# Optimization experiments

Measured on AMD Instinct MI355X. Metric: run time of the kernel, lower is better.

## Reference

```python
import jax, jax.numpy as jnp
import numpy as np

NA = 100000
NB = 100000
N_REL = 6
REL_SRC = ['A', 'B', 'A', 'B', 'A', 'B']
REL_DST = ['B', 'A', 'A', 'B', 'B', 'A']
N_NODES = {'A': NA, 'B': NB}
H_DIM, OUT_DIM, N_BASES, N_EDGES = 64, 16, 4, 500000


def setup_inputs() -> dict:
    key = jax.random.key(0)
    ks = jax.random.split(key, 16)
    inp = {
        'embed_A': jax.random.normal(ks[0], (NA, H_DIM), jnp.float32) * 0.1,
        'embed_B': jax.random.normal(ks[1], (NB, H_DIM), jnp.float32) * 0.1,
        'bias0': jnp.zeros((H_DIM,), jnp.float32),
        'w_comp1': jax.random.normal(ks[2], (N_REL, N_BASES), jnp.float32) * 0.5,
        'basis1': jax.random.normal(ks[3], (N_BASES, H_DIM, H_DIM), jnp.float32) * (1.0 / np.sqrt(H_DIM)),
        'bias1': jnp.zeros((H_DIM,), jnp.float32),
        'w_comp2': jax.random.normal(ks[4], (N_REL, N_BASES), jnp.float32) * 0.5,
        'basis2': jax.random.normal(ks[5], (N_BASES, H_DIM, OUT_DIM), jnp.float32) * (1.0 / np.sqrt(H_DIM)),
        'bias2': jnp.zeros((OUT_DIM,), jnp.float32),
    }
    for r in range(N_REL):
        inp[f'src_r{r}'] = jax.random.randint(ks[6 + r], (N_EDGES,), 0, N_NODES[REL_SRC[r]], jnp.int32)
        inp[f'dst_r{r}'] = jax.random.randint(jax.random.fold_in(ks[6 + r], 7), (N_EDGES,), 0, N_NODES[REL_DST[r]], jnp.int32)
    return inp


def _hetero_conv(h, W_rels, bias, edges, out_dim, activation):
    # h: dict ntype -> [N, d_in]; W_rels: None or [n_rel, d_in, d_out]
    out = {nt: jnp.zeros((N_NODES[nt], out_dim), h['A'].dtype) for nt in N_NODES}
    for r in range(N_REL):
        src_t, dst_t = REL_SRC[r], REL_DST[r]
        src, dst = edges[r]
        x = h[src_t] if W_rels is None else h[src_t] @ W_rels[r]  # [N_src, d_out]
        msg = x[src]  # gather: [E, d_out]
        n_dst = N_NODES[dst_t]
        agg = jax.ops.segment_sum(msg, dst, num_segments=n_dst)
        deg = jax.ops.segment_sum(jnp.ones((msg.shape[0],), msg.dtype), dst, num_segments=n_dst)
        out[dst_t] = out[dst_t] + agg / jnp.maximum(deg, 1.0)[:, None]  # norm='right'
    out = {nt: out[nt] + bias for nt in out}
    if activation is not None:
        out = {nt: activation(out[nt]) for nt in out}
    return out


def reference(embed_A, embed_B, bias0, w_comp1, basis1, bias1, w_comp2, basis2, bias2,
              src_r0, dst_r0, src_r1, dst_r1, src_r2, dst_r2,
              src_r3, dst_r3, src_r4, dst_r4, src_r5, dst_r5):
    edges = [(src_r0, dst_r0), (src_r1, dst_r1), (src_r2, dst_r2),
             (src_r3, dst_r3), (src_r4, dst_r4), (src_r5, dst_r5)]
    h = {'A': embed_A, 'B': embed_B}
    # layer 0: weight=False -> pure normalized aggregation + bias + relu
    h = _hetero_conv(h, None, bias0, edges, H_DIM, jax.nn.relu)
    # hidden layer with basis-decomposed weights
    W1 = jnp.einsum('rb,bio->rio', w_comp1, basis1)
    h = _hetero_conv(h, W1, bias1, edges, H_DIM, jax.nn.relu)
    # output layer, no activation
    W2 = jnp.einsum('rb,bio->rio', w_comp2, basis2)
    h = _hetero_conv(h, W2, bias2, edges, OUT_DIM, None)
    return h['A']  # logits for category node type
```

## Files before the change

kernel.cpp:

```cpp
#include <hip/hip_runtime.h>

#define NN 100000
#define EE 500000
#define DD 64
#define OD 16
#define NR 6
#define NBASE 4
#define BSH 10
#define NBK 98
#define SBLK 128
#define FLATN (NBK * SBLK)
#define STCAP 5632
#define DBIN 64
#define LROW 100

struct Edges { const int* src[NR]; const int* dst[NR]; };

typedef __attribute__((ext_vector_type(8))) short bf16x8;
typedef __attribute__((ext_vector_type(4))) float f32x4;

__device__ __forceinline__ float bf2f(ushort u) {
    union { unsigned int i; float f; } v; v.i = ((unsigned int)u) << 16; return v.f;
}
__device__ __forceinline__ ushort f2bf(float f) {
    unsigned int x = __float_as_uint(f);
    unsigned int r = (x + 0x7fffu + ((x >> 16) & 1u)) >> 16;
    return (ushort)r;
}
__device__ __forceinline__ void bfpair(unsigned int u, float& lo, float& hi) {
    lo = __uint_as_float(u << 16);
    hi = __uint_as_float(u & 0xffff0000u);
}

__global__ __launch_bounds__(256) void build_w_kernel(
    const float* __restrict__ wc1, const float* __restrict__ b1,
    const float* __restrict__ wc2, const float* __restrict__ b2,
    ushort* __restrict__ Wp1, ushort* __restrict__ Wp2)
{
    int idx = blockIdx.x * blockDim.x + threadIdx.x;
    const int n1 = NR * DD * DD;
    const int n2 = NR * DD * OD;
    if (idx < n1) {
        int r = idx >> 12, rem = idx & 4095;
        int i = rem >> 6, o = rem & 63;
        float s = 0.f;
        #pragma unroll
        for (int b = 0; b < NBASE; ++b) s += wc1[r * NBASE + b] * b1[b * 4096 + rem];
        Wp1[(((size_t)(r * 8 + (i >> 3)) * 64 + o) << 3) + (i & 7)] = f2bf(s);
    } else if (idx < n1 + n2) {
        int j = idx - n1;
        int r = j >> 10, rem = j & 1023;
        int i = rem >> 4, o = rem & 15;
        float s = 0.f;
        #pragma unroll
        for (int b = 0; b < NBASE; ++b) s += wc2[r * NBASE + b] * b2[b * 1024 + rem];
        Wp2[(((size_t)(r * 8 + (i >> 3)) * 16 + o) << 3) + (i & 7)] = f2bf(s);
    }
}

__global__ __launch_bounds__(256) void count_kernel(Edges ep, int* __restrict__ cnt_mat)
{
    __shared__ int h[NBK];
    int r = blockIdx.y, blk = blockIdx.x;
    const int* __restrict__ dst = ep.dst[r];
    const int chunk = (EE + SBLK - 1) / SBLK;
    int e0 = blk * chunk, e1 = min(e0 + chunk, EE);
    for (int i = threadIdx.x; i < NBK; i += 256) h[i] = 0;
    __syncthreads();
    for (int e = e0 + threadIdx.x; e < e1; e += 256)
        atomicAdd(&h[dst[e] >> BSH], 1);
    __syncthreads();
    for (int b = threadIdx.x; b < NBK; b += 256)
        cnt_mat[r * FLATN + b * SBLK + blk] = h[b];
}

__global__ __launch_bounds__(1024) void flat_scan_kernel(
    const int* __restrict__ cnt_mat, int* __restrict__ off_flat, int* __restrict__ bbase)
{
    __shared__ int wsum[16];
    const int TPE = 13;
    int r = blockIdx.x;
    int tid = threadIdx.x, lane = tid & 63, wid = tid >> 6;
    int base = tid * TPE;
    int v[TPE];
    int s = 0;
    #pragma unroll
    for (int j = 0; j < TPE; ++j) {
        int i = base + j;
        v[j] = (i < FLATN) ? cnt_mat[r * FLATN + i] : 0;
        s += v[j];
    }
    int si = s;
    #pragma unroll
    for (int off = 1; off < 64; off <<= 1) {
        int t = __shfl_up(si, off);
        if (lane >= off) si += t;
    }
    if (lane == 63) wsum[wid] = si;
    __syncthreads();
    if (wid == 0) {
        int ws = (lane < 16) ? wsum[lane] : 0;
        #pragma unroll
        for (int off = 1; off < 16; off <<= 1) {
            int t = __shfl_up(ws, off);
            if (lane >= off) ws += t;
        }
        if (lane < 16) wsum[lane] = ws;
    }
    __syncthreads();
    int texcl = (wid > 0 ? wsum[wid - 1] : 0) + (si - s);
    int part = 0;
    #pragma unroll
    for (int j = 0; j < TPE; ++j) {
        int i = base + j;
        if (i < FLATN) {
            int o = texcl + part;
            off_flat[r * FLATN + i] = o;
            if ((i & (SBLK - 1)) == 0) bbase[r * (NBK + 1) + (i >> 7)] = o;
        }
        part += v[j];
    }
    if (tid == 0) bbase[r * (NBK + 1) + NBK] = EE;
}

__global__ __launch_bounds__(256) void scatter2_kernel(
    Edges ep, const int* __restrict__ off_flat, unsigned int* __restrict__ ebuf)
{
    __shared__ int goff[NBK];
    __shared__ int lcnt[NBK];
    int r = blockIdx.y, blk = blockIdx.x;
    const int* __restrict__ src = ep.src[r];
    const int* __restrict__ dst = ep.dst[r];
    unsigned int* eb = ebuf + (size_t)r * EE;
    const int chunk = (EE + SBLK - 1) / SBLK;
    int e0 = blk * chunk, e1 = min(e0 + chunk, EE);
    if (threadIdx.x < NBK) {
        goff[threadIdx.x] = off_flat[r * FLATN + threadIdx.x * SBLK + blk];
        lcnt[threadIdx.x] = 0;
    }
    __syncthreads();
    for (int e = e0 + threadIdx.x; e < e1; e += 256) {
        int d = dst[e];
        int b = d >> BSH;
        int pos = goff[b] + atomicAdd(&lcnt[b], 1);
        eb[pos] = (unsigned int)src[e] | ((unsigned int)(d & 1023) << 17);
    }
}

__global__ __launch_bounds__(256) void csr_fine_kernel(
    const unsigned int* __restrict__ ebuf, const int* __restrict__ bbase,
    int* __restrict__ row_ptr, float* __restrict__ inv_deg, int* __restrict__ col_idx)
{
    __shared__ int nh[1024];
    __shared__ int nb[1024];
    __shared__ int wsum4[4];
    __shared__ int stage[STCAP];
    int r = blockIdx.y, b = blockIdx.x;
    int tid = threadIdx.x, lane = tid & 63, wid = tid >> 6;
    int gb = bbase[r * (NBK + 1) + b];
    int ge = bbase[r * (NBK + 1) + b + 1];
    int cnt = ge - gb;
    if (cnt > STCAP) cnt = STCAP;
    const unsigned int* eb = ebuf + (size_t)r * EE + gb;
    #pragma unroll
    for (int j = 0; j < 4; ++j) nh[tid * 4 + j] = 0;
    __syncthreads();
    for (int i = tid; i < cnt; i += 256)
        atomicAdd(&nh[(eb[i] >> 17) & 1023], 1);
    __syncthreads();
    int v0 = nh[tid * 4 + 0], v1 = nh[tid * 4 + 1], v2 = nh[tid * 4 + 2], v3 = nh[tid * 4 + 3];
    int s = v0 + v1 + v2 + v3;
    int si = s;
    #pragma unroll
    for (int off = 1; off < 64; off <<= 1) {
        int t = __shfl_up(si, off);
        if (lane >= off) si += t;
    }
    if (lane == 63) wsum4[wid] = si;
    __syncthreads();
    if (tid == 0) {
        int a = 0;
        #pragma unroll
        for (int k = 0; k < 4; ++k) { int t = wsum4[k]; wsum4[k] = a; a += t; }
    }
    __syncthreads();
    int texcl = wsum4[wid] + (si - s);
    int p0 = texcl, p1 = p0 + v0, p2 = p1 + v1, p3 = p2 + v2;
    nb[tid * 4 + 0] = p0; nb[tid * 4 + 1] = p1; nb[tid * 4 + 2] = p2; nb[tid * 4 + 3] = p3;
    {
        int node0 = b * 1024 + tid * 4;
        int pj[4] = { p0, p1, p2, p3 };
        int vj[4] = { v0, v1, v2, v3 };
        #pragma unroll
        for (int j = 0; j < 4; ++j) {
            int node = node0 + j;
            if (node < NN) {
                row_ptr[r * (NN + 1) + node] = gb + pj[j];
                inv_deg[r * NN + node] = 1.0f / (float)(vj[j] > 1 ? vj[j] : 1);
            }
        }
    }
    if (b == NBK - 1 && tid == 0) row_ptr[r * (NN + 1) + NN] = EE;
    #pragma unroll
    for (int j = 0; j < 4; ++j) nh[tid * 4 + j] = 0;
    __syncthreads();
    for (int i = tid; i < cnt; i += 256) {
        unsigned int w = eb[i];
        int loc = (w >> 17) & 1023;
        int pos = nb[loc] + atomicAdd(&nh[loc], 1);
        stage[pos] = (int)(w & 0x1ffffu);
    }
    __syncthreads();
    int* co = col_idx + (size_t)r * EE + gb;
    for (int i = tid; i < cnt; i += 256) co[i] = stage[i];
}

__device__ __forceinline__ int sdeg(int vr, int n, const int* __restrict__ rp)
{
    if (vr == 0)
        return (rp[1 * (NN + 1) + n + 1] - rp[1 * (NN + 1) + n])
             + (rp[2 * (NN + 1) + n + 1] - rp[2 * (NN + 1) + n])
             + (rp[5 * (NN + 1) + n + 1] - rp[5 * (NN + 1) + n]);
    return (rp[0 * (NN + 1) + n + 1] - rp[0 * (NN + 1) + n])
         + (rp[3 * (NN + 1) + n + 1] - rp[3 * (NN + 1) + n])
         + (rp[4 * (NN + 1) + n + 1] - rp[4 * (NN + 1) + n]);
}

__global__ __launch_bounds__(256) void bsort_kernel(
    const int* __restrict__ row_ptr, int* __restrict__ perm, int* __restrict__ iperm)
{
    __shared__ int h[DBIN];
    __shared__ int base_[DBIN];
    int vr = blockIdx.y, b = blockIdx.x;
    int n0 = b * 1024;
    int cnt = min(1024, NN - n0);
    int tid = threadIdx.x;
    if (tid < DBIN) h[tid] = 0;
    __syncthreads();
    int bin[4];
    #pragma unroll
    for (int j = 0; j < 4; ++j) {
        int i = tid + j * 256;
        if (i < cnt) {
            bin[j] = min(sdeg(vr, n0 + i, row_ptr), DBIN - 1);
            atomicAdd(&h[bin[j]], 1);
        } else bin[j] = -1;
    }
    __syncthreads();
    if (tid < 64) {
        int v = h[tid];
        int s = v;
        #pragma unroll
        for (int off = 1; off < 64; off <<= 1) {
            int t = __shfl_up(s, off);
            if (tid >= off) s += t;
        }
        base_[tid] = s - v;
        h[tid] = 0;
    }
    __syncthreads();
    #pragma unroll
    for (int j = 0; j < 4; ++j) {
        if (bin[j] >= 0) {
            int n = n0 + tid + j * 256;
            int pos = n0 + base_[bin[j]] + atomicAdd(&h[bin[j]], 1);
            perm[vr * NN + pos] = n;
            iperm[vr * NN + n] = pos;
        }
    }
}

__global__ __launch_bounds__(256) void translate_kernel(
    const int* __restrict__ iperm, int* __restrict__ col_idx)
{
    const int srcSide[NR] = {0, 1, 0, 1, 0, 1};
    int r = blockIdx.y;
    const int* ip = iperm + srcSide[r] * NN;
    int* ci = col_idx + (size_t)r * EE;
    for (int e = blockIdx.x * 256 + threadIdx.x; e < EE; e += gridDim.x * 256)
        ci[e] = ip[ci[e]];
}

__global__ __launch_bounds__(256) void cvtp_kernel(
    const float* __restrict__ inA, const float* __restrict__ inB,
    const int* __restrict__ perm, ushort* __restrict__ outA, ushort* __restrict__ outB)
{
    int side = blockIdx.y;
    int t = blockIdx.x * 256 + threadIdx.x;
    if (t >= NN * 8) return;
    int idx = t >> 3, j = t & 7;
    int n = perm[side * NN + idx];
    const float* in = side ? inB : inA;
    ushort* out = side ? outB : outA;
    float4 v0 = ((const float4*)in)[n * 16 + j * 2];
    float4 v1 = ((const float4*)in)[n * 16 + j * 2 + 1];
    int4 o;
    o.x = (int)((unsigned int)f2bf(v0.x) | ((unsigned int)f2bf(v0.y) << 16));
    o.y = (int)((unsigned int)f2bf(v0.z) | ((unsigned int)f2bf(v0.w) << 16));
    o.z = (int)((unsigned int)f2bf(v1.x) | ((unsigned int)f2bf(v1.y) << 16));
    o.w = (int)((unsigned int)f2bf(v1.z) | ((unsigned int)f2bf(v1.w) << 16));
    *(int4*)(out + (size_t)idx * DD + j * 8) = o;
}

__global__ __launch_bounds__(256) void layer0_kernel(
    const ushort* __restrict__ eA, const ushort* __restrict__ eB,
    const int* __restrict__ row_ptr, const int* __restrict__ col_idx,
    const float* __restrict__ inv_deg, const int* __restrict__ perm,
    const float* __restrict__ bias, ushort* __restrict__ hA, ushort* __restrict__ hB)
{
    int side = blockIdx.y;
    const int relT[2][3] = { {1, 2, 5}, {0, 3, 4} };
    int tid = threadIdx.x;
    int wid = tid >> 6, lane = tid & 63;
    int grp = lane >> 3, sub = lane & 7;
    int idx = blockIdx.x * 32 + wid * 8 + grp;
    bool valid = (idx < NN);
    int n = valid ? perm[side * NN + idx] : 0;
    float acc[8];
    {
        float4 b0 = *(const float4*)(bias + sub * 8);
        float4 b1 = *(const float4*)(bias + sub * 8 + 4);
        acc[0] = b0.x; acc[1] = b0.y; acc[2] = b0.z; acc[3] = b0.w;
        acc[4] = b1.x; acc[5] = b1.y; acc[6] = b1.z; acc[7] = b1.w;
    }
    #pragma unroll
    for (int ks = 0; ks < 3; ++ks) {
        int r = relT[side][ks];
        const ushort* F = ((side == 0) == (ks == 1)) ? eA : eB;
        const int* rp = row_ptr + r * (NN + 1);
        const int* ci = col_idx + (size_t)r * EE;
        int s = valid ? rp[n] : 0;
        int e = valid ? rp[n + 1] : 0;
        float a0 = 0.f, a1 = 0.f, a2 = 0.f, a3 = 0.f, a4 = 0.f, a5 = 0.f, a6 = 0.f, a7 = 0.f;
        int t = s;
        for (; t + 2 <= e; t += 2) {
            int c0 = ci[t], c1 = ci[t + 1];
            int4 u = *(const int4*)(F + (size_t)c0 * DD + sub * 8);
            int4 w = *(const int4*)(F + (size_t)c1 * DD + sub * 8);
            float l, h;
            bfpair((unsigned int)u.x, l, h); a0 += l; a1 += h;
            bfpair((unsigned int)u.y, l, h); a2 += l; a3 += h;
            bfpair((unsigned int)u.z, l, h); a4 += l; a5 += h;
            bfpair((unsigned int)u.w, l, h); a6 += l; a7 += h;
            bfpair((unsigned int)w.x, l, h); a0 += l; a1 += h;
            bfpair((unsigned int)w.y, l, h); a2 += l; a3 += h;
            bfpair((unsigned int)w.z, l, h); a4 += l; a5 += h;
            bfpair((unsigned int)w.w, l, h); a6 += l; a7 += h;
        }
        if (t < e) {
            int4 u = *(const int4*)(F + (size_t)ci[t] * DD + sub * 8);
            float l, h;
            bfpair((unsigned int)u.x, l, h); a0 += l; a1 += h;
            bfpair((unsigned int)u.y, l, h); a2 += l; a3 += h;
            bfpair((unsigned int)u.z, l, h); a4 += l; a5 += h;
            bfpair((unsigned int)u.w, l, h); a6 += l; a7 += h;
        }
        float inv = valid ? inv_deg[r * NN + n] : 0.f;
        acc[0] += a0 * inv; acc[1] += a1 * inv; acc[2] += a2 * inv; acc[3] += a3 * inv;
        acc[4] += a4 * inv; acc[5] += a5 * inv; acc[6] += a6 * inv; acc[7] += a7 * inv;
    }
    if (valid) {
        ushort* h = side ? hB : hA;
        int4 o;
        o.x = (int)((unsigned int)f2bf(fmaxf(acc[0], 0.f)) | ((unsigned int)f2bf(fmaxf(acc[1], 0.f)) << 16));
        o.y = (int)((unsigned int)f2bf(fmaxf(acc[2], 0.f)) | ((unsigned int)f2bf(fmaxf(acc[3], 0.f)) << 16));
        o.z = (int)((unsigned int)f2bf(fmaxf(acc[4], 0.f)) | ((unsigned int)f2bf(fmaxf(acc[5], 0.f)) << 16));
        o.w = (int)((unsigned int)f2bf(fmaxf(acc[6], 0.f)) | ((unsigned int)f2bf(fmaxf(acc[7], 0.f)) << 16));
        *(int4*)(h + (size_t)idx * DD + sub * 8) = o;
    }
}

__global__ __launch_bounds__(256) void layer1_fused_kernel(
    const ushort* __restrict__ h0A, const ushort* __restrict__ h0B,
    const int* __restrict__ row_ptr, const int* __restrict__ col_idx,
    const float* __restrict__ inv_deg, const int* __restrict__ perm,
    const ushort* __restrict__ Wp, const float* __restrict__ bias,
    ushort* __restrict__ h1A, ushort* __restrict__ h1B)
{
    __shared__ unsigned int sZ[32 * LROW];
    int side = blockIdx.y;
    const int relT[2][3] = { {1, 2, 5}, {0, 3, 4} };
    int tid = threadIdx.x;
    int wid = tid >> 6, lane = tid & 63;
    int grp = lane >> 3, sub = lane & 7;
    int ln = wid * 8 + grp;
    int idx0 = blockIdx.x * 32;
    int idx = idx0 + ln;
    bool valid = (idx < NN);
    int n = valid ? perm[side * NN + idx] : 0;
    #pragma unroll
    for (int ks = 0; ks < 3; ++ks) {
        int r = relT[side][ks];
        const ushort* F = ((side == 0) == (ks == 1)) ? h0A : h0B;
        const int* rp = row_ptr + r * (NN + 1);
        const int* ci = col_idx + (size_t)r * EE;
        int s = valid ? rp[n] : 0;
        int e = valid ? rp[n + 1] : 0;
        float a0 = 0.f, a1 = 0.f, a2 = 0.f, a3 = 0.f, a4 = 0.f, a5 = 0.f, a6 = 0.f, a7 = 0.f;
        int t = s;
        for (; t + 2 <= e; t += 2) {
            int c0 = ci[t], c1 = ci[t + 1];
            int4 u = *(const int4*)(F + (size_t)c0 * DD + sub * 8);
            int4 w = *(const int4*)(F + (size_t)c1 * DD + sub * 8);
            float l, h;
            bfpair((unsigned int)u.x, l, h); a0 += l; a1 += h;
            bfpair((unsigned int)u.y, l, h); a2 += l; a3 += h;
            bfpair((unsigned int)u.z, l, h); a4 += l; a5 += h;
            bfpair((unsigned int)u.w, l, h); a6 += l; a7 += h;
            bfpair((unsigned int)w.x, l, h); a0 += l; a1 += h;
            bfpair((unsigned int)w.y, l, h); a2 += l; a3 += h;
            bfpair((unsigned int)w.z, l, h); a4 += l; a5 += h;
            bfpair((unsigned int)w.w, l, h); a6 += l; a7 += h;
        }
        if (t < e) {
            int4 u = *(const int4*)(F + (size_t)ci[t] * DD + sub * 8);
            float l, h;
            bfpair((unsigned int)u.x, l, h); a0 += l; a1 += h;
            bfpair((unsigned int)u.y, l, h); a2 += l; a3 += h;
            bfpair((unsigned int)u.z, l, h); a4 += l; a5 += h;
            bfpair((unsigned int)u.w, l, h); a6 += l; a7 += h;
        }
        float inv = valid ? inv_deg[r * NN + n] : 0.f;
        int4 o;
        o.x = (int)((unsigned int)f2bf(a0 * inv) | ((unsigned int)f2bf(a1 * inv) << 16));
        o.y = (int)((unsigned int)f2bf(a2 * inv) | ((unsigned int)f2bf(a3 * inv) << 16));
        o.z = (int)((unsigned int)f2bf(a4 * inv) | ((unsigned int)f2bf(a5 * inv) << 16));
        o.w = (int)((unsigned int)f2bf(a6 * inv) | ((unsigned int)f2bf(a7 * inv) << 16));
        *(int4*)&sZ[ln * LROW + ks * 32 + sub * 4] = o;
    }
    __syncthreads();
    int q = lane & 15, p = lane >> 4;
    int base16 = (wid >> 1) * 16, cb = (wid & 1) * 32;
    f32x4 acc0 = {0.f, 0.f, 0.f, 0.f};
    f32x4 acc1 = {0.f, 0.f, 0.f, 0.f};
    #pragma unroll
    for (int ks = 0; ks < 3; ++ks) {
        int rel = relT[side][ks];
        #pragma unroll
        for (int tt = 0; tt < 2; ++tt) {
            int4 t4 = *(const int4*)&sZ[(base16 + q) * LROW + (ks * 2 + tt) * 16 + p * 4];
            bf16x8 a = *(const bf16x8*)&t4;
            const ushort* wb = Wp + (((size_t)(rel * 8 + tt * 4 + p) * 64 + cb + q) << 3);
            bf16x8 b0 = *(const bf16x8*)wb;
            bf16x8 b1 = *(const bf16x8*)(wb + 16 * 8);
            acc0 = __builtin_amdgcn_mfma_f32_16x16x32_bf16(a, b0, acc0, 0, 0, 0);
            acc1 = __builtin_amdgcn_mfma_f32_16x16x32_bf16(a, b1, acc1, 0, 0, 0);
        }
    }
    __syncthreads();
    ushort* sC = (ushort*)sZ;
    {
        float bv0 = bias[cb + q], bv1 = bias[cb + 16 + q];
        #pragma unroll
        for (int v = 0; v < 4; ++v) {
            int row = base16 + p * 4 + v;
            sC[row * 64 + cb + q]      = f2bf(fmaxf(acc0[v] + bv0, 0.f));
            sC[row * 64 + cb + 16 + q] = f2bf(fmaxf(acc1[v] + bv1, 0.f));
        }
    }
    __syncthreads();
    ushort* out = side ? h1B : h1A;
    int row = tid >> 3, c8 = (tid & 7) * 8;
    if (idx0 + row < NN)
        *(int4*)(out + (size_t)(idx0 + row) * DD + c8) = *(const int4*)(sC + row * 64 + c8);
}

__global__ __launch_bounds__(256) void layer2_fused_kernel(
    const ushort* __restrict__ h1A, const ushort* __restrict__ h1B,
    const int* __restrict__ row_ptr, const int* __restrict__ col_idx,
    const float* __restrict__ inv_deg, const int* __restrict__ perm,
    const ushort* __restrict__ Wp, const float* __restrict__ bias,
    float* __restrict__ out)
{
    __shared__ unsigned int sZ[32 * LROW];
    const int relT[3] = { 1, 2, 5 };
    int tid = threadIdx.x;
    int wid = tid >> 6, lane = tid & 63;
    int grp = lane >> 3, sub = lane & 7;
    int ln = wid * 8 + grp;
    int idx0 = blockIdx.x * 32;
    int idx = idx0 + ln;
    bool valid = (idx < NN);
    int n = valid ? perm[idx] : 0;
    #pragma unroll
    for (int ks = 0; ks < 3; ++ks) {
        int r = relT[ks];
        const ushort* F = (ks == 1) ? h1A : h1B;
        const int* rp = row_ptr + r * (NN + 1);
        const int* ci = col_idx + (size_t)r * EE;
        int s = valid ? rp[n] : 0;
        int e = valid ? rp[n + 1] : 0;
        float a0 = 0.f, a1 = 0.f, a2 = 0.f, a3 = 0.f, a4 = 0.f, a5 = 0.f, a6 = 0.f, a7 = 0.f;
        int t = s;
        for (; t + 2 <= e; t += 2) {
            int c0 = ci[t], c1 = ci[t + 1];
            int4 u = *(const int4*)(F + (size_t)c0 * DD + sub * 8);
            int4 w = *(const int4*)(F + (size_t)c1 * DD + sub * 8);
            float l, h;
            bfpair((unsigned int)u.x, l, h); a0 += l; a1 += h;
            bfpair((unsigned int)u.y, l, h); a2 += l; a3 += h;
            bfpair((unsigned int)u.z, l, h); a4 += l; a5 += h;
            bfpair((unsigned int)u.w, l, h); a6 += l; a7 += h;
            bfpair((unsigned int)w.x, l, h); a0 += l; a1 += h;
            bfpair((unsigned int)w.y, l, h); a2 += l; a3 += h;
            bfpair((unsigned int)w.z, l, h); a4 += l; a5 += h;
            bfpair((unsigned int)w.w, l, h); a6 += l; a7 += h;
        }
        if (t < e) {
            int4 u = *(const int4*)(F + (size_t)ci[t] * DD + sub * 8);
            float l, h;
            bfpair((unsigned int)u.x, l, h); a0 += l; a1 += h;
            bfpair((unsigned int)u.y, l, h); a2 += l; a3 += h;
            bfpair((unsigned int)u.z, l, h); a4 += l; a5 += h;
            bfpair((unsigned int)u.w, l, h); a6 += l; a7 += h;
        }
        float inv = valid ? inv_deg[r * NN + n] : 0.f;
        int4 o;
        o.x = (int)((unsigned int)f2bf(a0 * inv) | ((unsigned int)f2bf(a1 * inv) << 16));
        o.y = (int)((unsigned int)f2bf(a2 * inv) | ((unsigned int)f2bf(a3 * inv) << 16));
        o.z = (int)((unsigned int)f2bf(a4 * inv) | ((unsigned int)f2bf(a5 * inv) << 16));
        o.w = (int)((unsigned int)f2bf(a6 * inv) | ((unsigned int)f2bf(a7 * inv) << 16));
        *(int4*)&sZ[ln * LROW + ks * 32 + sub * 4] = o;
    }
    __syncthreads();
    if (wid < 2) {
        int q = lane & 15, p = lane >> 4;
        int base16 = wid * 16;
        f32x4 acc = {0.f, 0.f, 0.f, 0.f};
        #pragma unroll
        for (int ks = 0; ks < 3; ++ks) {
            int rel = relT[ks];
            #pragma unroll
            for (int tt = 0; tt < 2; ++tt) {
                int4 t4 = *(const int4*)&sZ[(base16 + q) * LROW + (ks * 2 + tt) * 16 + p * 4];
                bf16x8 a = *(const bf16x8*)&t4;
                bf16x8 b = *(const bf16x8*)(Wp + (((size_t)(rel * 8 + tt * 4 + p) * 16 + q) << 3));
                acc = __builtin_amdgcn_mfma_f32_16x16x32_bf16(a, b, acc, 0, 0, 0);
            }
        }
        float bv = bias[q];
        #pragma unroll
        for (int v = 0; v < 4; ++v) {
            int ridx = idx0 + base16 + p * 4 + v;
            if (ridx < NN) {
                int pn = perm[ridx];
                out[(size_t)pn * OD + q] = acc[v] + bv;
            }
        }
    }
}

extern "C" void kernel_launch(void* const* d_in, const int* in_sizes, int n_in,
                              void* d_out, int out_size, void* d_ws, size_t ws_size,
                              hipStream_t stream)
{
    const float* embA  = (const float*)d_in[0];
    const float* embB  = (const float*)d_in[1];
    const float* bias0 = (const float*)d_in[2];
    const float* wc1   = (const float*)d_in[3];
    const float* b1    = (const float*)d_in[4];
    const float* bias1 = (const float*)d_in[5];
    const float* wc2   = (const float*)d_in[6];
    const float* b2    = (const float*)d_in[7];
    const float* bias2 = (const float*)d_in[8];

    Edges ep;
    for (int r = 0; r < NR; ++r) {
        ep.src[r] = (const int*)d_in[9 + 2 * r];
        ep.dst[r] = (const int*)d_in[10 + 2 * r];
    }

    char* ws = (char*)d_ws;
    size_t off = 0;
    auto alloc = [&](size_t bytes) {
        void* p = ws + off;
        off = (off + bytes + 255) & ~(size_t)255;
        return p;
    };
    ushort* Wp1     = (ushort*)alloc((size_t)NR * 8 * 64 * 8 * 2);
    ushort* Wp2     = (ushort*)alloc((size_t)NR * 8 * 16 * 8 * 2);
    int*    cnt_mat = (int*)   alloc((size_t)NR * FLATN * 4);
    int*    off_fl  = (int*)   alloc((size_t)NR * FLATN * 4);
    int*    bbase   = (int*)   alloc((size_t)NR * (NBK + 1) * 4);
    int*    row_ptr = (int*)   alloc((size_t)NR * (NN + 1) * 4);
    float*  inv_deg = (float*) alloc((size_t)NR * NN * 4);
    int*    col_idx = (int*)   alloc((size_t)NR * EE * 4);
    int*    perm    = (int*)   alloc((size_t)2 * NN * 4);
    int*    iperm   = (int*)   alloc((size_t)2 * NN * 4);
    ushort* reg1    = (ushort*)alloc((size_t)2 * NN * DD * 2);
    ushort* h0pA    = (ushort*)alloc((size_t)NN * DD * 2);
    ushort* h0pB    = (ushort*)alloc((size_t)NN * DD * 2);
    (void)ws_size;

    unsigned int* ebuf  = (unsigned int*)reg1;
    ushort*       embpA = reg1;
    ushort*       embpB = reg1 + (size_t)NN * DD;
    ushort*       h1pA  = reg1;
    ushort*       h1pB  = reg1 + (size_t)NN * DD;

    int nw = NR * DD * DD + NR * DD * OD;
    build_w_kernel<<<(nw + 255) / 256, 256, 0, stream>>>(wc1, b1, wc2, b2, Wp1, Wp2);

    count_kernel<<<dim3(SBLK, NR), 256, 0, stream>>>(ep, cnt_mat);
    flat_scan_kernel<<<NR, 1024, 0, stream>>>(cnt_mat, off_fl, bbase);
    scatter2_kernel<<<dim3(SBLK, NR), 256, 0, stream>>>(ep, off_fl, ebuf);
    csr_fine_kernel<<<dim3(NBK, NR), 256, 0, stream>>>(ebuf, bbase, row_ptr, inv_deg, col_idx);

    bsort_kernel<<<dim3(NBK, 2), 256, 0, stream>>>(row_ptr, perm, iperm);
    translate_kernel<<<dim3(64, NR), 256, 0, stream>>>(iperm, col_idx);
    cvtp_kernel<<<dim3((NN * 8 + 255) / 256, 2), 256, 0, stream>>>(
        embA, embB, perm, embpA, embpB);

    int agx = (NN + 31) / 32;

    layer0_kernel<<<dim3(agx, 2), 256, 0, stream>>>(
        embpA, embpB, row_ptr, col_idx, inv_deg, perm, bias0, h0pA, h0pB);

    layer1_fused_kernel<<<dim3(agx, 2), 256, 0, stream>>>(
        h0pA, h0pB, row_ptr, col_idx, inv_deg, perm, Wp1, bias1, h1pA, h1pB);

    layer2_fused_kernel<<<agx, 256, 0, stream>>>(
        h1pA, h1pB, row_ptr, col_idx, inv_deg, perm, Wp2, bias2, (float*)d_out);
}
```

Measured before the change: 311.6 us.

## Project layer-2 features before gathering to shrink gather width

Layer 1 now multiplies its 64-wide output tile by the per-relation layer-2 weights inside the same kernel, writing 16-wide bf16 projections for the three relations that feed node type A. Layer 2 becomes a pure gather of 16-wide rows with degree normalisation and bias, instead of gathering 64-wide rows and then running an MFMA. This relies on the transform commuting with the normalised sum, and it cuts gathered bytes per edge by a factor of four. The cost is extra MFMA work and y2 writes in layer 1, plus an added bf16 rounding of the projected values.

```diff
diff --git a/kernel.cpp b/kernel.cpp
--- a/kernel.cpp
+++ b/kernel.cpp
@@ -374,8 +374,8 @@
     const ushort* __restrict__ h0A, const ushort* __restrict__ h0B,
     const int* __restrict__ row_ptr, const int* __restrict__ col_idx,
     const float* __restrict__ inv_deg, const int* __restrict__ perm,
-    const ushort* __restrict__ Wp, const float* __restrict__ bias,
-    ushort* __restrict__ h1A, ushort* __restrict__ h1B)
+    const ushort* __restrict__ Wp, const ushort* __restrict__ Wp2,
+    const float* __restrict__ bias, ushort* __restrict__ y2)
 {
     __shared__ unsigned int sZ[32 * LROW];
     int side = blockIdx.y;
@@ -459,95 +459,72 @@
         }
     }
     __syncthreads();
-    ushort* out = side ? h1B : h1A;
-    int row = tid >> 3, c8 = (tid & 7) * 8;
-    if (idx0 + row < NN)
-        *(int4*)(out + (size_t)(idx0 + row) * DD + c8) = *(const int4*)(sC + row * 64 + c8);
-}
-
-__global__ __launch_bounds__(256) void layer2_fused_kernel(
-    const ushort* __restrict__ h1A, const ushort* __restrict__ h1B,
+    int yb16, rel2_, slot;
+    bool doy;
+    if (side == 0) { doy = (wid < 2); yb16 = wid * 16;        rel2_ = 2;                    slot = 1; }
+    else           { doy = true;      yb16 = (wid & 1) * 16;  rel2_ = (wid >> 1) ? 5 : 1;   slot = (wid >> 1) ? 2 : 0; }
+    if (doy) {
+        f32x4 yacc = {0.f, 0.f, 0.f, 0.f};
+        #pragma unroll
+        for (int tt = 0; tt < 2; ++tt) {
+            bf16x8 a = *(const bf16x8*)(sC + (yb16 + q) * 64 + tt * 32 + p * 8);
+            bf16x8 b = *(const bf16x8*)(Wp2 + (((size_t)(rel2_ * 8 + tt * 4 + p) * 16 + q) << 3));
+            yacc = __builtin_amdgcn_mfma_f32_16x16x32_bf16(a, b, yacc, 0, 0, 0);
+        }
+        ushort* Y = y2 + (size_t)slot * NN * OD;
+        #pragma unroll
+        for (int v = 0; v < 4; ++v) {
+            int row = yb16 + p * 4 + v;
+            if (idx0 + row < NN) Y[(size_t)(idx0 + row) * OD + q] = f2bf(yacc[v]);
+        }
+    }
+}
+
+__global__ __launch_bounds__(256) void layer2_gather_kernel(
+    const ushort* __restrict__ y2,
     const int* __restrict__ row_ptr, const int* __restrict__ col_idx,
     const float* __restrict__ inv_deg, const int* __restrict__ perm,
-    const ushort* __restrict__ Wp, const float* __restrict__ bias,
-    float* __restrict__ out)
-{
-    __shared__ unsigned int sZ[32 * LROW];
-    const int relT[3] = { 1, 2, 5 };
+    const float* __restrict__ bias, float* __restrict__ out)
+{
+    const int rr0 = 1, rr1 = 2, rr2 = 5;
+    const ushort* Y0 = y2;
+    const ushort* Y1 = y2 + (size_t)NN * OD;
+    const ushort* Y2 = y2 + (size_t)2 * NN * OD;
     int tid = threadIdx.x;
     int wid = tid >> 6, lane = tid & 63;
     int grp = lane >> 3, sub = lane & 7;
-    int ln = wid * 8 + grp;
-    int idx0 = blockIdx.x * 32;
-    int idx = idx0 + ln;
-    bool valid = (idx < NN);
-    int n = valid ? perm[idx] : 0;
+    int idx = blockIdx.x * 32 + wid * 8 + grp;
+    if (idx >= NN) return;
+    int n = perm[idx];
+    float o0 = 0.f, o1 = 0.f;
     #pragma unroll
     for (int ks = 0; ks < 3; ++ks) {
-        int r = relT[ks];
-        const ushort* F = (ks == 1) ? h1A : h1B;
+        int r = (ks == 0) ? rr0 : ((ks == 1) ? rr1 : rr2);
+        const ushort* Y = (ks == 0) ? Y0 : ((ks == 1) ? Y1 : Y2);
         const int* rp = row_ptr + r * (NN + 1);
         const int* ci = col_idx + (size_t)r * EE;
-        int s = valid ? rp[n] : 0;
-        int e = valid ? rp[n + 1] : 0;
-        float a0 = 0.f, a1 = 0.f, a2 = 0.f, a3 = 0.f, a4 = 0.f, a5 = 0.f, a6 = 0.f, a7 = 0.f;
+        int s = rp[n], e = rp[n + 1];
+        float a0 = 0.f, a1 = 0.f;
         int t = s;
         for (; t + 2 <= e; t += 2) {
-            int c0 = ci[t], c1 = ci[t + 1];
-            int4 u = *(const int4*)(F + (size_t)c0 * DD + sub * 8);
-            int4 w = *(const int4*)(F + (size_t)c1 * DD + sub * 8);
+            unsigned int u = *(const unsigned int*)(Y + (size_t)ci[t] * OD + sub * 2);
+            unsigned int w = *(const unsigned int*)(Y + (size_t)ci[t + 1] * OD + sub * 2);
             float l, h;
-            bfpair((unsigned int)u.x, l, h); a0 += l; a1 += h;
-            bfpair((unsigned int)u.y, l, h); a2 += l; a3 += h;
-            bfpair((unsigned int)u.z, l, h); a4 += l; a5 += h;
-            bfpair((unsigned int)u.w, l, h); a6 += l; a7 += h;
-            bfpair((unsigned int)w.x, l, h); a0 += l; a1 += h;
-            bfpair((unsigned int)w.y, l, h); a2 += l; a3 += h;
-            bfpair((unsigned int)w.z, l, h); a4 += l; a5 += h;
-            bfpair((unsigned int)w.w, l, h); a6 += l; a7 += h;
+            bfpair(u, l, h); a0 += l; a1 += h;
+            bfpair(w, l, h); a0 += l; a1 += h;
         }
         if (t < e) {
-            int4 u = *(const int4*)(F + (size_t)ci[t] * DD + sub * 8);
+            unsigned int u = *(const unsigned int*)(Y + (size_t)ci[t] * OD + sub * 2);
             float l, h;
-            bfpair((unsigned int)u.x, l, h); a0 += l; a1 += h;
-            bfpair((unsigned int)u.y, l, h); a2 += l; a3 += h;
-            bfpair((unsigned int)u.z, l, h); a4 += l; a5 += h;
-            bfpair((unsigned int)u.w, l, h); a6 += l; a7 += h;
-        }
-        float inv = valid ? inv_deg[r * NN + n] : 0.f;
-        int4 o;
-        o.x = (int)((unsigned int)f2bf(a0 * inv) | ((unsigned int)f2bf(a1 * inv) << 16));
-        o.y = (int)((unsigned int)f2bf(a2 * inv) | ((unsigned int)f2bf(a3 * inv) << 16));
-        o.z = (int)((unsigned int)f2bf(a4 * inv) | ((unsigned int)f2bf(a5 * inv) << 16));
-        o.w = (int)((unsigned int)f2bf(a6 * inv) | ((unsigned int)f2bf(a7 * inv) << 16));
-        *(int4*)&sZ[ln * LROW + ks * 32 + sub * 4] = o;
-    }
-    __syncthreads();
-    if (wid < 2) {
-        int q = lane & 15, p = lane >> 4;
-        int base16 = wid * 16;
-        f32x4 acc = {0.f, 0.f, 0.f, 0.f};
-        #pragma unroll
-        for (int ks = 0; ks < 3; ++ks) {
-            int rel = relT[ks];
-            #pragma unroll
-            for (int tt = 0; tt < 2; ++tt) {
-                int4 t4 = *(const int4*)&sZ[(base16 + q) * LROW + (ks * 2 + tt) * 16 + p * 4];
-                bf16x8 a = *(const bf16x8*)&t4;
-                bf16x8 b = *(const bf16x8*)(Wp + (((size_t)(rel * 8 + tt * 4 + p) * 16 + q) << 3));
-                acc = __builtin_amdgcn_mfma_f32_16x16x32_bf16(a, b, acc, 0, 0, 0);
-            }
-        }
-        float bv = bias[q];
-        #pragma unroll
-        for (int v = 0; v < 4; ++v) {
-            int ridx = idx0 + base16 + p * 4 + v;
-            if (ridx < NN) {
-                int pn = perm[ridx];
-                out[(size_t)pn * OD + q] = acc[v] + bv;
-            }
-        }
-    }
+            bfpair(u, l, h); a0 += l; a1 += h;
+        }
+        float inv = inv_deg[r * NN + n];
+        o0 += a0 * inv; o1 += a1 * inv;
+    }
+    float2 ov;
+    ov.x = o0 + bias[sub * 2];
+    ov.y = o1 + bias[sub * 2 + 1];
+    *(float2*)(out + (size_t)n * OD + sub * 2) = ov;
 }
 
 extern "C" void kernel_launch(void* const* d_in, const int* in_sizes, int n_in,
@@ -595,8 +572,7 @@
     unsigned int* ebuf  = (unsigned int*)reg1;
     ushort*       embpA = reg1;
     ushort*       embpB = reg1 + (size_t)NN * DD;
-    ushort*       h1pA  = reg1;
-    ushort*       h1pB  = reg1 + (size_t)NN * DD;
+    ushort*       y2buf = reg1;
 
     int nw = NR * DD * DD + NR * DD * OD;
     build_w_kernel<<<(nw + 255) / 256, 256, 0, stream>>>(wc1, b1, wc2, b2, Wp1, Wp2);
@@ -617,8 +593,8 @@
         embpA, embpB, row_ptr, col_idx, inv_deg, perm, bias0, h0pA, h0pB);
 
     layer1_fused_kernel<<<dim3(agx, 2), 256, 0, stream>>>(
-        h0pA, h0pB, row_ptr, col_idx, inv_deg, perm, Wp1, bias1, h1pA, h1pB);
-
-    layer2_fused_kernel<<<agx, 256, 0, stream>>>(
-        h1pA, h1pB, row_ptr, col_idx, inv_deg, perm, Wp2, bias2, (float*)d_out);
-}
+        h0pA, h0pB, row_ptr, col_idx, inv_deg, perm, Wp1, Wp2, bias1, y2buf);
+
+    layer2_gather_kernel<<<agx, 256, 0, stream>>>(
+        y2buf, row_ptr, col_idx, inv_deg, perm, bias2, (float*)d_out);
+}
```

Result: faster. 300.7 us (-3.5%).
